# Kernel tuning notes

Hardware: AMD Instinct MI355X
Metric: run time of the kernel (lower is better)

## Reference

```python
import jax, jax.numpy as jnp
import numpy as np

EPS = 1e-7
MAX_NORM = 1.0 - 1e-5  # Poincare ball (c=1) projection radius
NUM_NODES = 50000
NUM_EDGES = 800000
NUM_GRAPHS = 512
D_IN = 64
D_H = 64
D_OUT = 16


def _norm(x):
    return jnp.clip(jnp.linalg.norm(x, axis=-1, keepdims=True), EPS)


def expmap0(u):
    n = _norm(u)
    return jnp.tanh(n) * u / n


def logmap0(x):
    n = _norm(x)
    nc = jnp.clip(n, EPS, MAX_NORM)
    return jnp.arctanh(nc) * x / n


def proj(x):
    n = _norm(x)
    return jnp.where(n > MAX_NORM, x * (MAX_NORM / n), x)


def mobius_add(x, y):
    x2 = jnp.sum(x * x, axis=-1, keepdims=True)
    y2 = jnp.sum(y * y, axis=-1, keepdims=True)
    xy = jnp.sum(x * y, axis=-1, keepdims=True)
    num = (1.0 + 2.0 * xy + y2) * x + (1.0 - x2) * y
    den = jnp.clip(1.0 + 2.0 * xy + x2 * y2, EPS)
    return num / den


def hyp_linear(x, W, b):
    # mobius matvec + hyperbolic bias add
    h = proj(expmap0(logmap0(x) @ W.T))
    hb = proj(expmap0(b))
    return proj(mobius_add(h, hb))


def hyp_agg(x, src, dst, num_nodes):
    # mean aggregation of neighbor messages in the tangent space at the origin
    xt = logmap0(x)                                   # [N, d]
    msg = xt[src]                                     # [E, d] gather
    s = jax.ops.segment_sum(msg, dst, num_segments=num_nodes)
    cnt = jax.ops.segment_sum(jnp.ones((msg.shape[0],), xt.dtype), dst,
                              num_segments=num_nodes)
    agg = s / jnp.clip(cnt, 1.0)[:, None]
    return proj(expmap0(agg))


def hyp_act(x, act):
    return proj(expmap0(act(logmap0(x))))


def hgcn_layer(x, W, b, src, dst, num_nodes, act):
    h = hyp_linear(x, W, b)
    h = hyp_agg(h, src, dst, num_nodes)
    if act is not None:
        h = hyp_act(h, act)
    return h


def setup_inputs() -> dict:
    key = jax.random.key(0)
    ks = jax.random.split(key, 12)
    x = jax.random.normal(ks[0], (NUM_NODES, D_IN), jnp.float32) * 0.1
    edge_index = jax.random.randint(ks[1], (2, NUM_EDGES), 0, NUM_NODES, jnp.int64 if jax.config.jax_enable_x64 else jnp.int32)
    batch = jnp.sort(jax.random.randint(ks[2], (NUM_NODES,), 0, NUM_GRAPHS))
    def w(k, o, i):
        return jax.random.normal(k, (o, i), jnp.float32) * (1.0 / np.sqrt(i))
    return {
        "x": x,
        "W1": w(ks[3], D_H, D_IN), "b1": jnp.zeros((D_H,), jnp.float32),
        "W2": w(ks[4], D_H, D_H),  "b2": jnp.zeros((D_H,), jnp.float32),
        "W3": w(ks[5], D_H, D_H),  "b3": jnp.zeros((D_H,), jnp.float32),
        "W4": w(ks[6], D_OUT, D_H), "b4": jnp.zeros((D_OUT,), jnp.float32),
        "edge_index": edge_index,
        "batch": batch,
    }


def reference(x, W1, b1, W2, b2, W3, b3, W4, b4, edge_index, batch):
    act = lambda v: jax.nn.leaky_relu(v, 0.2)
    n = x.shape[0]
    src, dst = edge_index[0], edge_index[1]
    h = proj(expmap0(x))
    h = hgcn_layer(h, W1, b1, src, dst, n, act)
    h = hgcn_layer(h, W2, b2, src, dst, n, act)
    h = hgcn_layer(h, W3, b3, src, dst, n, None)
    t = logmap0(h)
    # global mean pool over graphs (eval-mode dropout = identity)
    s = jax.ops.segment_sum(t, batch, num_segments=NUM_GRAPHS)
    cnt = jax.ops.segment_sum(jnp.ones((n,), t.dtype), batch, num_segments=NUM_GRAPHS)
    pooled = s / jnp.clip(cnt, 1.0)[:, None]            # [G, d]
    h = proj(expmap0(pooled))
    out = hyp_linear(h, W4, b4)                          # HNNLayer, no activation
    return out
```

## Files before the change

### kernel.cpp

```cpp
#include <hip/hip_runtime.h>
#include <hip/hip_fp16.h>

#define EPSF 1e-7f
#define MAXNORM (1.0f - 1e-5f)

__device__ __forceinline__ float rsum64(float v) {
#pragma unroll
  for (int m = 32; m; m >>= 1) v += __shfl_xor(v, m, 64);
  return v;
}
__device__ __forceinline__ float rsum16(float v) {
#pragma unroll
  for (int m = 8; m; m >>= 1) v += __shfl_xor(v, m, 64);
  return v;
}
__device__ __forceinline__ float gr8(float v) {
  v += __shfl_xor(v, 1, 64);
  v += __shfl_xor(v, 2, 64);
  v += __shfl_xor(v, 4, 64);
  return v;
}

__device__ __forceinline__ float frcp(float x) { return __builtin_amdgcn_rcpf(x); }
__device__ __forceinline__ float fsqrt_(float x) { return __builtin_amdgcn_sqrtf(x); }
__device__ __forceinline__ float tanh_fast(float x) {
  x = fminf(x, 20.f);
  float e = __builtin_amdgcn_exp2f(x * 2.88539008178f);
  return (e - 1.f) * frcp(e + 1.f);
}
__device__ __forceinline__ float atanh_fast(float x) {
  return 0.34657359028f * __builtin_amdgcn_logf((1.f + x) * frcp(1.f - x));
}
__device__ __forceinline__ float lp_exp_log_scale(float nu) {
  float te = tanh_fast(nu);
  float tec = fminf(fmaxf(te, EPSF), MAXNORM);
  return atanh_fast(tec) * frcp(fmaxf(te, EPSF)) * te * frcp(nu);
}

__device__ __forceinline__ float4 ld4(const float* p) {
  return *reinterpret_cast<const float4*>(p);
}

__device__ __forceinline__ void hb_from_b(const float* __restrict__ b, int sub,
                                          float hb8[8], float& hb2) {
  float4 b0 = ld4(b + sub * 8), b1 = ld4(b + sub * 8 + 4);
  float bb8[8] = {b0.x, b0.y, b0.z, b0.w, b1.x, b1.y, b1.z, b1.w};
  float p = 0.f;
#pragma unroll
  for (int j = 0; j < 8; ++j) p = fmaf(bb8[j], bb8[j], p);
  p = gr8(p);
  float nb = fmaxf(fsqrt_(p), EPSF);
  float cb = fminf(tanh_fast(nb), MAXNORM);
  float kb = cb * frcp(nb);
#pragma unroll
  for (int j = 0; j < 8; ++j) hb8[j] = kb * bb8[j];
  hb2 = cb * cb;
}

__device__ __forceinline__ void gather8h(const unsigned short* __restrict__ csr,
                                         const __half* __restrict__ xtp,
                                         int r0, int deg, int g, int sub,
                                         float acc[8]) {
  const uint4* xt4 = reinterpret_cast<const uint4*>(xtp);
  int lb = g << 3;
  int cur = (sub < deg) ? (int)csr[r0 + sub] : 0;
  for (int j0 = 0; j0 < deg; j0 += 8) {
    int nj = j0 + 8;
    int nxt = (nj + sub < deg) ? (int)csr[r0 + nj + sub] : 0;
#pragma unroll
    for (int m = 0; m < 8; ++m) {
      int idx = __shfl(cur, lb + m, 64);
      float msk = (j0 + m < deg) ? 1.f : 0.f;
      union { uint4 u; __half2 h[4]; } U;
      U.u = xt4[(size_t)idx * 8 + sub];
      float2 f0 = __half22float2(U.h[0]);
      float2 f1 = __half22float2(U.h[1]);
      float2 f2 = __half22float2(U.h[2]);
      float2 f3 = __half22float2(U.h[3]);
      acc[0] = fmaf(msk, f0.x, acc[0]); acc[1] = fmaf(msk, f0.y, acc[1]);
      acc[2] = fmaf(msk, f1.x, acc[2]); acc[3] = fmaf(msk, f1.y, acc[3]);
      acc[4] = fmaf(msk, f2.x, acc[4]); acc[5] = fmaf(msk, f2.y, acc[5]);
      acc[6] = fmaf(msk, f3.x, acc[6]); acc[7] = fmaf(msk, f3.y, acc[7]);
    }
    cur = nxt;
  }
}

__device__ __forceinline__ void st8h(__half* __restrict__ xt, int node, int sub,
                                     const float o[8]) {
  union { uint4 u; __half2 h[4]; } U;
  U.h[0] = __floats2half2_rn(o[0], o[1]);
  U.h[1] = __floats2half2_rn(o[2], o[3]);
  U.h[2] = __floats2half2_rn(o[4], o[5]);
  U.h[3] = __floats2half2_rn(o[6], o[7]);
  reinterpret_cast<uint4*>(xt)[(size_t)node * 8 + sub] = U.u;
}

__device__ __forceinline__ void linear_tail8(
    const float* __restrict__ Wl, float* __restrict__ sc, int g, int sub,
    int lane, const float t2[8], const float hb8[8], float hb2, float out8[8]) {
  float4* sw = reinterpret_cast<float4*>(sc + g * 68 + sub * 8);
  sw[0] = make_float4(t2[0], t2[1], t2[2], t2[3]);
  sw[1] = make_float4(t2[4], t2[5], t2[6], t2[7]);
  float y[8] = {0.f, 0.f, 0.f, 0.f, 0.f, 0.f, 0.f, 0.f};
  const float4* Wrow = reinterpret_cast<const float4*>(Wl + lane * 68);
#pragma unroll
  for (int q = 0; q < 16; ++q) {
    float4 w = Wrow[q];
#pragma unroll
    for (int g2 = 0; g2 < 8; ++g2) {
      float4 tq = *reinterpret_cast<const float4*>(sc + g2 * 68 + q * 4);
      y[g2] = fmaf(w.x, tq.x, fmaf(w.y, tq.y, fmaf(w.z, tq.z, fmaf(w.w, tq.w, y[g2]))));
    }
  }
#pragma unroll
  for (int g2 = 0; g2 < 8; ++g2) sc[g2 * 68 + lane] = y[g2];
  float4 r0 = *reinterpret_cast<const float4*>(sc + g * 68 + sub * 8);
  float4 r1 = *reinterpret_cast<const float4*>(sc + g * 68 + sub * 8 + 4);
  float yv[8] = {r0.x, r0.y, r0.z, r0.w, r1.x, r1.y, r1.z, r1.w};
  float p1 = 0.f, p2 = 0.f;
#pragma unroll
  for (int j = 0; j < 8; ++j) {
    p1 = fmaf(yv[j], yv[j], p1);
    p2 = fmaf(yv[j], hb8[j], p2);
  }
  p1 = gr8(p1); p2 = gr8(p2);
  float ny = fmaxf(fsqrt_(p1), EPSF);
  float cy = fminf(tanh_fast(ny), MAXNORM);
  float k = cy * frcp(ny);
  float xy = k * p2;
  float x2 = cy * cy;
  float aa = 1.f + 2.f * xy + hb2;
  float cc = 1.f - x2;
  float den = fmaxf(1.f + 2.f * xy + x2 * hb2, EPSF);
  float rd = frcp(den);
  float nr2 = (aa * aa * x2 + 2.f * aa * cc * xy + cc * cc * hb2) * rd * rd;
  float nr = fmaxf(fsqrt_(nr2), EPSF);
  float s = atanh_fast(fminf(nr, MAXNORM)) * frcp(nr);
  float sk = s * rd;
#pragma unroll
  for (int j = 0; j < 8; ++j) out8[j] = sk * (aa * k * yv[j] + cc * hb8[j]);
}

__global__ void __launch_bounds__(256) k_histg(
    const int* __restrict__ dst, int* __restrict__ deg8, int* __restrict__ rank,
    int E, int N, const int* __restrict__ batch, float* __restrict__ cntg,
    int G, int nbE) {
  if ((int)blockIdx.x < nbE) {
    int e = blockIdx.x * 256 + threadIdx.x;
    if (e >= E) return;
    int c = (e >> 8) & 7;
    rank[e] = atomicAdd(&deg8[(size_t)c * N + dst[e]], 1);
  } else {
    int g = (blockIdx.x - nbE) * 256 + threadIdx.x;
    if (g >= G) return;
    int lo = 0, hi = N;
    while (lo < hi) { int mid = (lo + hi) >> 1; if (batch[mid] < g) lo = mid + 1; else hi = mid; }
    int lb = lo;
    lo = 0; hi = N; int g1 = g + 1;
    while (lo < hi) { int mid = (lo + hi) >> 1; if (batch[mid] < g1) lo = mid + 1; else hi = mid; }
    cntg[g] = (float)(lo - lb);
  }
}

__global__ void __launch_bounds__(256) k_scanAR(const int* __restrict__ deg8,
                                                int* __restrict__ offs8,
                                                int* __restrict__ locscan,
                                                int* __restrict__ partial, int N) {
  __shared__ int buf[256];
  int i = blockIdx.x * 256 + threadIdx.x;
  int s = 0;
  if (i < N) {
#pragma unroll
    for (int k = 0; k < 8; ++k) {
      int v = deg8[(size_t)k * N + i];
      offs8[(size_t)k * N + i] = s;
      s += v;
    }
  }
  int v0 = s;
  buf[threadIdx.x] = v0;
  __syncthreads();
#pragma unroll
  for (int off = 1; off < 256; off <<= 1) {
    int t = (threadIdx.x >= off) ? buf[threadIdx.x - off] : 0;
    __syncthreads();
    buf[threadIdx.x] += t;
    __syncthreads();
  }
  if (i < N) locscan[i] = buf[threadIdx.x] - v0;
  if (threadIdx.x == 255) partial[blockIdx.x] = buf[255];
}

__global__ void __launch_bounds__(256) k_scanB(int* __restrict__ partial, int nb) {
  __shared__ int buf[256];
  int carry = 0;
  for (int base = 0; base < nb; base += 256) {
    int i = base + threadIdx.x;
    int v = (i < nb) ? partial[i] : 0;
    buf[threadIdx.x] = v;
    __syncthreads();
#pragma unroll
    for (int off = 1; off < 256; off <<= 1) {
      int t = (threadIdx.x >= off) ? buf[threadIdx.x - off] : 0;
      __syncthreads();
      buf[threadIdx.x] += t;
      __syncthreads();
    }
    if (i < nb) partial[i] = carry + buf[threadIdx.x] - v;
    int total = buf[255];
    __syncthreads();
    carry += total;
  }
}

__global__ void __launch_bounds__(256) k_scanC(const int* __restrict__ locscan,
                                               const int* __restrict__ partial,
                                               int* __restrict__ rowptr, int N, int E) {
  int i = blockIdx.x * 256 + threadIdx.x;
  if (i < N) rowptr[i] = locscan[i] + partial[blockIdx.x];
  if (i == 0) rowptr[N] = E;
}

__global__ void __launch_bounds__(512) k_filllin(
    const int* __restrict__ src, const int* __restrict__ dst,
    const int* __restrict__ rank, const int* __restrict__ rowptr,
    const int* __restrict__ offs8, unsigned short* __restrict__ csr,
    int E, int N, int nbF,
    const float* __restrict__ x, const float* __restrict__ W,
    const float* __restrict__ b, __half* __restrict__ xt) {
  __shared__ __align__(16) float Wl[64 * 68];
  __shared__ __align__(16) float sc_all[8][8 * 68];
  if ((int)blockIdx.x < nbF) {
    int e = blockIdx.x * 512 + threadIdx.x;
    if (e >= E) return;
    int c = (e >> 8) & 7;
    int d = dst[e];
    csr[rowptr[d] + offs8[(size_t)c * N + d] + rank[e]] = (unsigned short)src[e];
    return;
  }
  int bb = blockIdx.x - nbF;
  int tid = threadIdx.x, wid = tid >> 6, lane = tid & 63;
  int g = lane >> 3, sub = lane & 7;
  for (int i = tid; i < 4096; i += 512) Wl[(i >> 6) * 68 + (i & 63)] = W[i];
  __syncthreads();
  float hb8[8], hb2;
  hb_from_b(b, sub, hb8, hb2);

  int slot = bb * 64 + wid * 8 + g;
  bool valid = slot < N;
  int node = valid ? slot : 0;
  const float* row = x + (size_t)node * 64 + sub * 8;
  float4 v0 = ld4(row), v1 = ld4(row + 4);
  float xa[8] = {v0.x, v0.y, v0.z, v0.w, v1.x, v1.y, v1.z, v1.w};
  float p = 0.f;
#pragma unroll
  for (int j = 0; j < 8; ++j) p = fmaf(xa[j], xa[j], p);
  p = gr8(p);
  float na = fmaxf(fsqrt_(p), EPSF);
  float sc1 = lp_exp_log_scale(na);
  float t2[8];
#pragma unroll
  for (int j = 0; j < 8; ++j) t2[j] = sc1 * xa[j];
  float out8[8];
  linear_tail8(Wl, sc_all[wid], g, sub, lane, t2, hb8, hb2, out8);
  if (valid) st8h(xt, node, sub, out8);
}

__global__ void __launch_bounds__(512) k_gatherlin(
    const int* __restrict__ rowptr, const unsigned short* __restrict__ csr,
    const __half* __restrict__ xtp, const float* __restrict__ W,
    const float* __restrict__ b, __half* __restrict__ xt, int N) {
  __shared__ __align__(16) float Wl[64 * 68];
  __shared__ __align__(16) float sc_all[8][8 * 68];
  int tid = threadIdx.x, wid = tid >> 6, lane = tid & 63;
  int g = lane >> 3, sub = lane & 7;
  for (int i = tid; i < 4096; i += 512) Wl[(i >> 6) * 68 + (i & 63)] = W[i];
  __syncthreads();
  float hb8[8], hb2;
  hb_from_b(b, sub, hb8, hb2);

  int slot = blockIdx.x * 64 + wid * 8 + g;
  bool valid = slot < N;
  int node = valid ? slot : 0;
  int r0 = rowptr[node];
  int deg = valid ? (rowptr[node + 1] - r0) : 0;
  float acc[8] = {0.f, 0.f, 0.f, 0.f, 0.f, 0.f, 0.f, 0.f};
  gather8h(csr, xtp, r0, deg, g, sub, acc);
  float rdeg = frcp(fmaxf((float)deg, 1.f));
  float u[8];
#pragma unroll
  for (int j = 0; j < 8; ++j) u[j] = acc[j] * rdeg;
  float p = 0.f, q = 0.f;
#pragma unroll
  for (int j = 0; j < 8; ++j) {
    float w = (u[j] < 0.f) ? 0.04f : 1.f;
    p = fmaf(u[j], u[j], p);
    q = fmaf(w * u[j], u[j], q);
  }
  p = gr8(p); q = gr8(q);
  float nu = fmaxf(fsqrt_(p), EPSF);
  float s1 = lp_exp_log_scale(nu);
  float nt = fmaxf(s1 * fsqrt_(q), EPSF);
  float f = lp_exp_log_scale(nt) * s1;
  float t2[8];
#pragma unroll
  for (int j = 0; j < 8; ++j) t2[j] = f * u[j] * ((u[j] < 0.f) ? 0.2f : 1.f);
  float out8[8];
  linear_tail8(Wl, sc_all[wid], g, sub, lane, t2, hb8, hb2, out8);
  if (valid) st8h(xt, node, sub, out8);
}

__global__ void __launch_bounds__(512) k_gpool(const int* __restrict__ rowptr,
                                               const unsigned short* __restrict__ csr,
                                               const __half* __restrict__ xtp,
                                               const int* __restrict__ batch,
                                               float* __restrict__ pooled, int N) {
  int tid = threadIdx.x, wid = tid >> 6, lane = tid & 63;
  int g = lane >> 3, sub = lane & 7;
  int slot = blockIdx.x * 64 + wid * 8 + g;
  bool valid = slot < N;
  int node = valid ? slot : 0;
  int r0 = rowptr[node];
  int deg = valid ? (rowptr[node + 1] - r0) : 0;
  float acc[8] = {0.f, 0.f, 0.f, 0.f, 0.f, 0.f, 0.f, 0.f};
  gather8h(csr, xtp, r0, deg, g, sub, acc);
  float rdeg = frcp(fmaxf((float)deg, 1.f));
  float u[8], p = 0.f;
#pragma unroll
  for (int j = 0; j < 8; ++j) {
    u[j] = acc[j] * rdeg;
    p = fmaf(u[j], u[j], p);
  }
  p = gr8(p);
  float nu = fmaxf(fsqrt_(p), EPSF);
  float s = lp_exp_log_scale(nu);
  float t8[8];
#pragma unroll
  for (int j = 0; j < 8; ++j) t8[j] = (valid ? s : 0.f) * u[j];
  int bs = batch[node];
  int b0 = __shfl(bs, 0, 64);
  bool uniform = __all(valid && bs == b0);
  if (uniform) {
#pragma unroll
    for (int j = 0; j < 8; ++j) {
      t8[j] += __shfl_xor(t8[j], 8, 64);
      t8[j] += __shfl_xor(t8[j], 16, 64);
      t8[j] += __shfl_xor(t8[j], 32, 64);
    }
    if (g == 0) {
#pragma unroll
      for (int j = 0; j < 8; ++j)
        atomicAdd(&pooled[(size_t)b0 * 64 + sub * 8 + j], t8[j]);
    }
  } else if (valid) {
#pragma unroll
    for (int j = 0; j < 8; ++j)
      atomicAdd(&pooled[(size_t)bs * 64 + sub * 8 + j], t8[j]);
  }
}

__global__ void __launch_bounds__(64) k_final(const float* __restrict__ pooled,
                                              const float* __restrict__ cntg,
                                              const float* __restrict__ W4,
                                              const float* __restrict__ b4,
                                              float* __restrict__ out, int G) {
  int g = blockIdx.x;
  int lane = threadIdx.x;
  float u = pooled[(size_t)g * 64 + lane] / fmaxf(cntg[g], 1.0f);
  float n = fmaxf(sqrtf(rsum64(u * u)), EPSF);
  float e = tanhf(n) * u / n;
  float ne = fmaxf(sqrtf(rsum64(e * e)), EPSF);
  if (ne > MAXNORM) e *= MAXNORM / ne;
  float nn = fmaxf(sqrtf(rsum64(e * e)), EPSF);
  float t = atanhf(fminf(nn, MAXNORM)) * e / nn;

  int row = lane & 15;
  float acc = 0.f;
#pragma unroll
  for (int k = 0; k < 64; ++k) {
    float tk = __shfl(t, k, 64);
    acc = fmaf(W4[row * 64 + k], tk, acc);
  }
  float ny = fmaxf(sqrtf(rsum16(acc * acc)), EPSF);
  float hy = tanhf(ny) * acc / ny;
  float nh = fmaxf(sqrtf(rsum16(hy * hy)), EPSF);
  if (nh > MAXNORM) hy *= MAXNORM / nh;
  float bb = b4[row];
  float nb = fmaxf(sqrtf(rsum16(bb * bb)), EPSF);
  float hb = tanhf(nb) * bb / nb;
  float nhb = fmaxf(sqrtf(rsum16(hb * hb)), EPSF);
  if (nhb > MAXNORM) hb *= MAXNORM / nhb;
  float x2 = rsum16(hy * hy);
  float y2 = rsum16(hb * hb);
  float xy = rsum16(hy * hb);
  float num = (1.f + 2.f * xy + y2) * hy + (1.f - x2) * hb;
  float den = fmaxf(1.f + 2.f * xy + x2 * y2, EPSF);
  float r = num / den;
  float nr = fmaxf(sqrtf(rsum16(r * r)), EPSF);
  if (nr > MAXNORM) r *= MAXNORM / nr;
  if (lane < 16) out[(size_t)g * 16 + lane] = r;
}

extern "C" void kernel_launch(void* const* d_in, const int* in_sizes, int n_in,
                              void* d_out, int out_size, void* d_ws, size_t ws_size,
                              hipStream_t stream) {
  const float* x  = (const float*)d_in[0];
  const float* W1 = (const float*)d_in[1];
  const float* b1 = (const float*)d_in[2];
  const float* W2 = (const float*)d_in[3];
  const float* b2 = (const float*)d_in[4];
  const float* W3 = (const float*)d_in[5];
  const float* b3 = (const float*)d_in[6];
  const float* W4 = (const float*)d_in[7];
  const float* b4 = (const float*)d_in[8];
  const int* ei   = (const int*)d_in[9];
  const int* batch = (const int*)d_in[10];

  int N = in_sizes[0] / 64;
  int E = in_sizes[9] / 2;
  int G = out_size / 16;
  const int* src = ei;
  const int* dst = ei + E;

  float* ws = (float*)d_ws;
  __half* xtA   = (__half*)ws;
  __half* xtB   = xtA + (size_t)N * 64;
  float* pooled = ws + (size_t)N * 64;
  float* cntg   = pooled + (size_t)G * 64;
  int* ip       = (int*)(cntg + G);
  int* deg8     = ip;
  int* offs8    = deg8 + (size_t)8 * N;
  int* locscan  = offs8 + (size_t)8 * N;
  int* rowptr   = locscan + N;
  int* partial  = rowptr + N + 1;
  int* rank     = partial + 256;
  unsigned short* csr = (unsigned short*)(rank + E);
  float* out = (float*)d_out;

  int nbE = (E + 255) / 256;
  int nbG = (G + 255) / 256;
  int nbN = (N + 255) / 256;
  int nbF = (E + 511) / 512;
  int nbL = (N + 63) / 64;

  hipMemsetAsync(deg8, 0, (size_t)8 * N * sizeof(int), stream);
  hipMemsetAsync(pooled, 0, (size_t)G * 64 * sizeof(float), stream);

  k_histg<<<nbE + nbG, 256, 0, stream>>>(dst, deg8, rank, E, N, batch, cntg, G, nbE);
  k_scanAR<<<nbN, 256, 0, stream>>>(deg8, offs8, locscan, partial, N);
  k_scanB<<<1, 256, 0, stream>>>(partial, nbN);
  k_scanC<<<nbN, 256, 0, stream>>>(locscan, partial, rowptr, N, E);
  k_filllin<<<nbF + nbL, 512, 0, stream>>>(src, dst, rank, rowptr, offs8, csr,
                                           E, N, nbF, x, W1, b1, xtA);
  k_gatherlin<<<nbL, 512, 0, stream>>>(rowptr, csr, xtA, W2, b2, xtB, N);
  k_gatherlin<<<nbL, 512, 0, stream>>>(rowptr, csr, xtB, W3, b3, xtA, N);
  k_gpool<<<nbL, 512, 0, stream>>>(rowptr, csr, xtA, batch, pooled, N);
  k_final<<<G, 64, 0, stream>>>(pooled, cntg, W4, b4, out, G);
}
```

Before: 174.3 us.

## Fuse all pipeline stages into one persistent cooperative kernel with grid syncs

Replaces the nine separate launches and two memsets (histogram, three-stage scan, CSR fill plus first linear, two gather-linear layers, pooling, final head) with a single cooperative kernel. The kernel uses grid-stride loops and grid.sync between stages, and the scan moves to 512-wide blocks. The aim is to remove per-launch overhead and the idle gaps between many small kernels. In exchange, the grid is capped at occupancy, which may reduce parallelism in the gather phases. Each grid barrier has its own cost, and the final head now runs on only a few waves.

```diff
diff --git a/kernel.cpp b/kernel.cpp
--- a/kernel.cpp
+++ b/kernel.cpp
@@ -1,5 +1,8 @@
 #include <hip/hip_runtime.h>
 #include <hip/hip_fp16.h>
+#include <hip/hip_cooperative_groups.h>
+
+namespace cg = cooperative_groups;
 
 #define EPSF 1e-7f
 #define MAXNORM (1.0f - 1e-5f)
@@ -142,286 +145,272 @@
   for (int j = 0; j < 8; ++j) out8[j] = sk * (aa * k * yv[j] + cc * hb8[j]);
 }
 
-__global__ void __launch_bounds__(256) k_histg(
-    const int* __restrict__ dst, int* __restrict__ deg8, int* __restrict__ rank,
-    int E, int N, const int* __restrict__ batch, float* __restrict__ cntg,
-    int G, int nbE) {
-  if ((int)blockIdx.x < nbE) {
-    int e = blockIdx.x * 256 + threadIdx.x;
-    if (e >= E) return;
-    int c = (e >> 8) & 7;
-    rank[e] = atomicAdd(&deg8[(size_t)c * N + dst[e]], 1);
-  } else {
-    int g = (blockIdx.x - nbE) * 256 + threadIdx.x;
-    if (g >= G) return;
-    int lo = 0, hi = N;
-    while (lo < hi) { int mid = (lo + hi) >> 1; if (batch[mid] < g) lo = mid + 1; else hi = mid; }
-    int lb = lo;
-    lo = 0; hi = N; int g1 = g + 1;
-    while (lo < hi) { int mid = (lo + hi) >> 1; if (batch[mid] < g1) lo = mid + 1; else hi = mid; }
-    cntg[g] = (float)(lo - lb);
-  }
-}
-
-__global__ void __launch_bounds__(256) k_scanAR(const int* __restrict__ deg8,
-                                                int* __restrict__ offs8,
-                                                int* __restrict__ locscan,
-                                                int* __restrict__ partial, int N) {
-  __shared__ int buf[256];
-  int i = blockIdx.x * 256 + threadIdx.x;
-  int s = 0;
-  if (i < N) {
-#pragma unroll
-    for (int k = 0; k < 8; ++k) {
-      int v = deg8[(size_t)k * N + i];
-      offs8[(size_t)k * N + i] = s;
-      s += v;
-    }
-  }
-  int v0 = s;
-  buf[threadIdx.x] = v0;
-  __syncthreads();
-#pragma unroll
-  for (int off = 1; off < 256; off <<= 1) {
-    int t = (threadIdx.x >= off) ? buf[threadIdx.x - off] : 0;
-    __syncthreads();
-    buf[threadIdx.x] += t;
-    __syncthreads();
-  }
-  if (i < N) locscan[i] = buf[threadIdx.x] - v0;
-  if (threadIdx.x == 255) partial[blockIdx.x] = buf[255];
-}
-
-__global__ void __launch_bounds__(256) k_scanB(int* __restrict__ partial, int nb) {
-  __shared__ int buf[256];
-  int carry = 0;
-  for (int base = 0; base < nb; base += 256) {
-    int i = base + threadIdx.x;
-    int v = (i < nb) ? partial[i] : 0;
-    buf[threadIdx.x] = v;
-    __syncthreads();
-#pragma unroll
-    for (int off = 1; off < 256; off <<= 1) {
-      int t = (threadIdx.x >= off) ? buf[threadIdx.x - off] : 0;
-      __syncthreads();
-      buf[threadIdx.x] += t;
-      __syncthreads();
-    }
-    if (i < nb) partial[i] = carry + buf[threadIdx.x] - v;
-    int total = buf[255];
-    __syncthreads();
-    carry += total;
-  }
-}
-
-__global__ void __launch_bounds__(256) k_scanC(const int* __restrict__ locscan,
-                                               const int* __restrict__ partial,
-                                               int* __restrict__ rowptr, int N, int E) {
-  int i = blockIdx.x * 256 + threadIdx.x;
-  if (i < N) rowptr[i] = locscan[i] + partial[blockIdx.x];
-  if (i == 0) rowptr[N] = E;
-}
-
-__global__ void __launch_bounds__(512) k_filllin(
-    const int* __restrict__ src, const int* __restrict__ dst,
-    const int* __restrict__ rank, const int* __restrict__ rowptr,
-    const int* __restrict__ offs8, unsigned short* __restrict__ csr,
-    int E, int N, int nbF,
-    const float* __restrict__ x, const float* __restrict__ W,
-    const float* __restrict__ b, __half* __restrict__ xt) {
+struct CoopArgs {
+  const int* src; const int* dst; const int* batch;
+  const float* x;
+  const float* W1; const float* b1;
+  const float* W2; const float* b2;
+  const float* W3; const float* b3;
+  const float* W4; const float* b4;
+  int* deg8; int* offs8; int* locscan; int* rowptr; int* partial;
+  int* rank; unsigned short* csr;
+  __half* xtA; __half* xtB;
+  float* pooled; float* cntg; float* out;
+  int N, E, G;
+};
+
+__global__ void __launch_bounds__(512) k_coop(CoopArgs a) {
+  cg::grid_group grid = cg::this_grid();
   __shared__ __align__(16) float Wl[64 * 68];
   __shared__ __align__(16) float sc_all[8][8 * 68];
-  if ((int)blockIdx.x < nbF) {
-    int e = blockIdx.x * 512 + threadIdx.x;
-    if (e >= E) return;
+  __shared__ int ibuf[512];
+
+  const int tid = threadIdx.x;
+  const int wid = tid >> 6, lane = tid & 63;
+  const int g = lane >> 3, sub = lane & 7;
+  const int gsz = gridDim.x;
+  const int N = a.N, E = a.E, G = a.G;
+  const int gstride = gsz * 512;
+  int gbase = blockIdx.x * 512 + tid;
+
+  for (int i = gbase; i < 8 * N; i += gstride) a.deg8[i] = 0;
+  for (int i = gbase; i < G * 64; i += gstride) a.pooled[i] = 0.f;
+  grid.sync();
+
+  for (int e = gbase; e < E; e += gstride) {
     int c = (e >> 8) & 7;
-    int d = dst[e];
-    csr[rowptr[d] + offs8[(size_t)c * N + d] + rank[e]] = (unsigned short)src[e];
-    return;
-  }
-  int bb = blockIdx.x - nbF;
-  int tid = threadIdx.x, wid = tid >> 6, lane = tid & 63;
-  int g = lane >> 3, sub = lane & 7;
-  for (int i = tid; i < 4096; i += 512) Wl[(i >> 6) * 68 + (i & 63)] = W[i];
+    a.rank[e] = atomicAdd(&a.deg8[(size_t)c * N + a.dst[e]], 1);
+  }
+  for (int gg = gbase; gg < G; gg += gstride) {
+    int lo = 0, hi = N;
+    while (lo < hi) { int mid = (lo + hi) >> 1; if (a.batch[mid] < gg) lo = mid + 1; else hi = mid; }
+    int lb2 = lo;
+    lo = 0; hi = N; int g1 = gg + 1;
+    while (lo < hi) { int mid = (lo + hi) >> 1; if (a.batch[mid] < g1) lo = mid + 1; else hi = mid; }
+    a.cntg[gg] = (float)(lo - lb2);
+  }
+  grid.sync();
+
+  int nbP = (N + 511) / 512;
+  for (int blk = blockIdx.x; blk < nbP; blk += gsz) {
+    int i = blk * 512 + tid;
+    int s = 0;
+    if (i < N) {
+#pragma unroll
+      for (int k = 0; k < 8; ++k) {
+        int v = a.deg8[(size_t)k * N + i];
+        a.offs8[(size_t)k * N + i] = s;
+        s += v;
+      }
+    }
+    int v0 = s;
+    __syncthreads();
+    ibuf[tid] = v0;
+    __syncthreads();
+#pragma unroll
+    for (int off = 1; off < 512; off <<= 1) {
+      int t = (tid >= off) ? ibuf[tid - off] : 0;
+      __syncthreads();
+      ibuf[tid] += t;
+      __syncthreads();
+    }
+    if (i < N) a.locscan[i] = ibuf[tid] - v0;
+    if (tid == 511) a.partial[blk] = ibuf[511];
+  }
+  grid.sync();
+
+  if (blockIdx.x == 0) {
+    int v = (tid < nbP) ? a.partial[tid] : 0;
+    ibuf[tid] = v;
+    __syncthreads();
+#pragma unroll
+    for (int off = 1; off < 512; off <<= 1) {
+      int t = (tid >= off) ? ibuf[tid - off] : 0;
+      __syncthreads();
+      ibuf[tid] += t;
+      __syncthreads();
+    }
+    if (tid < nbP) a.partial[tid] = ibuf[tid] - v;
+  }
+  grid.sync();
+
+  for (int blk = blockIdx.x; blk < nbP; blk += gsz) {
+    int i = blk * 512 + tid;
+    if (i < N) a.rowptr[i] = a.locscan[i] + a.partial[blk];
+  }
+  if (blockIdx.x == 0 && tid == 0) a.rowptr[N] = E;
+  grid.sync();
+
+  for (int e = gbase; e < E; e += gstride) {
+    int c = (e >> 8) & 7;
+    int d = a.dst[e];
+    a.csr[a.rowptr[d] + a.offs8[(size_t)c * N + d] + a.rank[e]] =
+        (unsigned short)a.src[e];
+  }
+  for (int i = tid; i < 4096; i += 512) Wl[(i >> 6) * 68 + (i & 63)] = a.W1[i];
   __syncthreads();
-  float hb8[8], hb2;
-  hb_from_b(b, sub, hb8, hb2);
-
-  int slot = bb * 64 + wid * 8 + g;
-  bool valid = slot < N;
-  int node = valid ? slot : 0;
-  const float* row = x + (size_t)node * 64 + sub * 8;
-  float4 v0 = ld4(row), v1 = ld4(row + 4);
-  float xa[8] = {v0.x, v0.y, v0.z, v0.w, v1.x, v1.y, v1.z, v1.w};
-  float p = 0.f;
-#pragma unroll
-  for (int j = 0; j < 8; ++j) p = fmaf(xa[j], xa[j], p);
-  p = gr8(p);
-  float na = fmaxf(fsqrt_(p), EPSF);
-  float sc1 = lp_exp_log_scale(na);
-  float t2[8];
-#pragma unroll
-  for (int j = 0; j < 8; ++j) t2[j] = sc1 * xa[j];
-  float out8[8];
-  linear_tail8(Wl, sc_all[wid], g, sub, lane, t2, hb8, hb2, out8);
-  if (valid) st8h(xt, node, sub, out8);
-}
-
-__global__ void __launch_bounds__(512) k_gatherlin(
-    const int* __restrict__ rowptr, const unsigned short* __restrict__ csr,
-    const __half* __restrict__ xtp, const float* __restrict__ W,
-    const float* __restrict__ b, __half* __restrict__ xt, int N) {
-  __shared__ __align__(16) float Wl[64 * 68];
-  __shared__ __align__(16) float sc_all[8][8 * 68];
-  int tid = threadIdx.x, wid = tid >> 6, lane = tid & 63;
-  int g = lane >> 3, sub = lane & 7;
-  for (int i = tid; i < 4096; i += 512) Wl[(i >> 6) * 68 + (i & 63)] = W[i];
-  __syncthreads();
-  float hb8[8], hb2;
-  hb_from_b(b, sub, hb8, hb2);
-
-  int slot = blockIdx.x * 64 + wid * 8 + g;
-  bool valid = slot < N;
-  int node = valid ? slot : 0;
-  int r0 = rowptr[node];
-  int deg = valid ? (rowptr[node + 1] - r0) : 0;
-  float acc[8] = {0.f, 0.f, 0.f, 0.f, 0.f, 0.f, 0.f, 0.f};
-  gather8h(csr, xtp, r0, deg, g, sub, acc);
-  float rdeg = frcp(fmaxf((float)deg, 1.f));
-  float u[8];
-#pragma unroll
-  for (int j = 0; j < 8; ++j) u[j] = acc[j] * rdeg;
-  float p = 0.f, q = 0.f;
-#pragma unroll
-  for (int j = 0; j < 8; ++j) {
-    float w = (u[j] < 0.f) ? 0.04f : 1.f;
-    p = fmaf(u[j], u[j], p);
-    q = fmaf(w * u[j], u[j], q);
-  }
-  p = gr8(p); q = gr8(q);
-  float nu = fmaxf(fsqrt_(p), EPSF);
-  float s1 = lp_exp_log_scale(nu);
-  float nt = fmaxf(s1 * fsqrt_(q), EPSF);
-  float f = lp_exp_log_scale(nt) * s1;
-  float t2[8];
-#pragma unroll
-  for (int j = 0; j < 8; ++j) t2[j] = f * u[j] * ((u[j] < 0.f) ? 0.2f : 1.f);
-  float out8[8];
-  linear_tail8(Wl, sc_all[wid], g, sub, lane, t2, hb8, hb2, out8);
-  if (valid) st8h(xt, node, sub, out8);
-}
-
-__global__ void __launch_bounds__(512) k_gpool(const int* __restrict__ rowptr,
-                                               const unsigned short* __restrict__ csr,
-                                               const __half* __restrict__ xtp,
-                                               const int* __restrict__ batch,
-                                               float* __restrict__ pooled, int N) {
-  int tid = threadIdx.x, wid = tid >> 6, lane = tid & 63;
-  int g = lane >> 3, sub = lane & 7;
-  int slot = blockIdx.x * 64 + wid * 8 + g;
-  bool valid = slot < N;
-  int node = valid ? slot : 0;
-  int r0 = rowptr[node];
-  int deg = valid ? (rowptr[node + 1] - r0) : 0;
-  float acc[8] = {0.f, 0.f, 0.f, 0.f, 0.f, 0.f, 0.f, 0.f};
-  gather8h(csr, xtp, r0, deg, g, sub, acc);
-  float rdeg = frcp(fmaxf((float)deg, 1.f));
-  float u[8], p = 0.f;
-#pragma unroll
-  for (int j = 0; j < 8; ++j) {
-    u[j] = acc[j] * rdeg;
-    p = fmaf(u[j], u[j], p);
-  }
-  p = gr8(p);
-  float nu = fmaxf(fsqrt_(p), EPSF);
-  float s = lp_exp_log_scale(nu);
-  float t8[8];
-#pragma unroll
-  for (int j = 0; j < 8; ++j) t8[j] = (valid ? s : 0.f) * u[j];
-  int bs = batch[node];
-  int b0 = __shfl(bs, 0, 64);
-  bool uniform = __all(valid && bs == b0);
-  if (uniform) {
-#pragma unroll
-    for (int j = 0; j < 8; ++j) {
-      t8[j] += __shfl_xor(t8[j], 8, 64);
-      t8[j] += __shfl_xor(t8[j], 16, 64);
-      t8[j] += __shfl_xor(t8[j], 32, 64);
-    }
-    if (g == 0) {
-#pragma unroll
-      for (int j = 0; j < 8; ++j)
-        atomicAdd(&pooled[(size_t)b0 * 64 + sub * 8 + j], t8[j]);
-    }
-  } else if (valid) {
-#pragma unroll
-    for (int j = 0; j < 8; ++j)
-      atomicAdd(&pooled[(size_t)bs * 64 + sub * 8 + j], t8[j]);
-  }
-}
-
-__global__ void __launch_bounds__(64) k_final(const float* __restrict__ pooled,
-                                              const float* __restrict__ cntg,
-                                              const float* __restrict__ W4,
-                                              const float* __restrict__ b4,
-                                              float* __restrict__ out, int G) {
-  int g = blockIdx.x;
-  int lane = threadIdx.x;
-  float u = pooled[(size_t)g * 64 + lane] / fmaxf(cntg[g], 1.0f);
-  float n = fmaxf(sqrtf(rsum64(u * u)), EPSF);
-  float e = tanhf(n) * u / n;
-  float ne = fmaxf(sqrtf(rsum64(e * e)), EPSF);
-  if (ne > MAXNORM) e *= MAXNORM / ne;
-  float nn = fmaxf(sqrtf(rsum64(e * e)), EPSF);
-  float t = atanhf(fminf(nn, MAXNORM)) * e / nn;
-
-  int row = lane & 15;
-  float acc = 0.f;
-#pragma unroll
-  for (int k = 0; k < 64; ++k) {
-    float tk = __shfl(t, k, 64);
-    acc = fmaf(W4[row * 64 + k], tk, acc);
-  }
-  float ny = fmaxf(sqrtf(rsum16(acc * acc)), EPSF);
-  float hy = tanhf(ny) * acc / ny;
-  float nh = fmaxf(sqrtf(rsum16(hy * hy)), EPSF);
-  if (nh > MAXNORM) hy *= MAXNORM / nh;
-  float bb = b4[row];
-  float nb = fmaxf(sqrtf(rsum16(bb * bb)), EPSF);
-  float hb = tanhf(nb) * bb / nb;
-  float nhb = fmaxf(sqrtf(rsum16(hb * hb)), EPSF);
-  if (nhb > MAXNORM) hb *= MAXNORM / nhb;
-  float x2 = rsum16(hy * hy);
-  float y2 = rsum16(hb * hb);
-  float xy = rsum16(hy * hb);
-  float num = (1.f + 2.f * xy + y2) * hy + (1.f - x2) * hb;
-  float den = fmaxf(1.f + 2.f * xy + x2 * y2, EPSF);
-  float r = num / den;
-  float nr = fmaxf(sqrtf(rsum16(r * r)), EPSF);
-  if (nr > MAXNORM) r *= MAXNORM / nr;
-  if (lane < 16) out[(size_t)g * 16 + lane] = r;
+  {
+    float hb8[8], hb2;
+    hb_from_b(a.b1, sub, hb8, hb2);
+    int nbL = (N + 63) / 64;
+    for (int blk = blockIdx.x; blk < nbL; blk += gsz) {
+      int slot = blk * 64 + wid * 8 + g;
+      bool valid = slot < N;
+      int node = valid ? slot : 0;
+      const float* row = a.x + (size_t)node * 64 + sub * 8;
+      float4 v0 = ld4(row), v1 = ld4(row + 4);
+      float xa[8] = {v0.x, v0.y, v0.z, v0.w, v1.x, v1.y, v1.z, v1.w};
+      float p = 0.f;
+#pragma unroll
+      for (int j = 0; j < 8; ++j) p = fmaf(xa[j], xa[j], p);
+      p = gr8(p);
+      float na = fmaxf(fsqrt_(p), EPSF);
+      float sc1 = lp_exp_log_scale(na);
+      float t2[8];
+#pragma unroll
+      for (int j = 0; j < 8; ++j) t2[j] = sc1 * xa[j];
+      float out8[8];
+      linear_tail8(Wl, sc_all[wid], g, sub, lane, t2, hb8, hb2, out8);
+      if (valid) st8h(a.xtA, node, sub, out8);
+    }
+  }
+  grid.sync();
+
+  for (int layer = 0; layer < 2; ++layer) {
+    const float* W = (layer == 0) ? a.W2 : a.W3;
+    const float* b = (layer == 0) ? a.b2 : a.b3;
+    const __half* xin = (layer == 0) ? a.xtA : a.xtB;
+    __half* xout = (layer == 0) ? a.xtB : a.xtA;
+    for (int i = tid; i < 4096; i += 512) Wl[(i >> 6) * 68 + (i & 63)] = W[i];
+    __syncthreads();
+    float hb8[8], hb2;
+    hb_from_b(b, sub, hb8, hb2);
+    int nbL = (N + 63) / 64;
+    for (int blk = blockIdx.x; blk < nbL; blk += gsz) {
+      int slot = blk * 64 + wid * 8 + g;
+      bool valid = slot < N;
+      int node = valid ? slot : 0;
+      int r0 = a.rowptr[node];
+      int deg = valid ? (a.rowptr[node + 1] - r0) : 0;
+      float acc[8] = {0.f, 0.f, 0.f, 0.f, 0.f, 0.f, 0.f, 0.f};
+      gather8h(a.csr, xin, r0, deg, g, sub, acc);
+      float rdeg = frcp(fmaxf((float)deg, 1.f));
+      float u[8];
+#pragma unroll
+      for (int j = 0; j < 8; ++j) u[j] = acc[j] * rdeg;
+      float p = 0.f, q = 0.f;
+#pragma unroll
+      for (int j = 0; j < 8; ++j) {
+        float w = (u[j] < 0.f) ? 0.04f : 1.f;
+        p = fmaf(u[j], u[j], p);
+        q = fmaf(w * u[j], u[j], q);
+      }
+      p = gr8(p); q = gr8(q);
+      float nu = fmaxf(fsqrt_(p), EPSF);
+      float s1 = lp_exp_log_scale(nu);
+      float nt = fmaxf(s1 * fsqrt_(q), EPSF);
+      float f = lp_exp_log_scale(nt) * s1;
+      float t2[8];
+#pragma unroll
+      for (int j = 0; j < 8; ++j) t2[j] = f * u[j] * ((u[j] < 0.f) ? 0.2f : 1.f);
+      float out8[8];
+      linear_tail8(Wl, sc_all[wid], g, sub, lane, t2, hb8, hb2, out8);
+      if (valid) st8h(xout, node, sub, out8);
+    }
+    grid.sync();
+  }
+
+  {
+    int nbL = (N + 63) / 64;
+    for (int blk = blockIdx.x; blk < nbL; blk += gsz) {
+      int slot = blk * 64 + wid * 8 + g;
+      bool valid = slot < N;
+      int node = valid ? slot : 0;
+      int r0 = a.rowptr[node];
+      int deg = valid ? (a.rowptr[node + 1] - r0) : 0;
+      float acc[8] = {0.f, 0.f, 0.f, 0.f, 0.f, 0.f, 0.f, 0.f};
+      gather8h(a.csr, a.xtA, r0, deg, g, sub, acc);
+      float rdeg = frcp(fmaxf((float)deg, 1.f));
+      float u[8], p = 0.f;
+#pragma unroll
+      for (int j = 0; j < 8; ++j) {
+        u[j] = acc[j] * rdeg;
+        p = fmaf(u[j], u[j], p);
+      }
+      p = gr8(p);
+      float nu = fmaxf(fsqrt_(p), EPSF);
+      float s = lp_exp_log_scale(nu);
+      float t8[8];
+#pragma unroll
+      for (int j = 0; j < 8; ++j) t8[j] = (valid ? s : 0.f) * u[j];
+      int bs = a.batch[node];
+      int b0 = __shfl(bs, 0, 64);
+      bool uniform = __all(valid && bs == b0);
+      if (uniform) {
+#pragma unroll
+        for (int j = 0; j < 8; ++j) {
+          t8[j] += __shfl_xor(t8[j], 8, 64);
+          t8[j] += __shfl_xor(t8[j], 16, 64);
+          t8[j] += __shfl_xor(t8[j], 32, 64);
+        }
+        if (g == 0) {
+#pragma unroll
+          for (int j = 0; j < 8; ++j)
+            atomicAdd(&a.pooled[(size_t)b0 * 64 + sub * 8 + j], t8[j]);
+        }
+      } else if (valid) {
+#pragma unroll
+        for (int j = 0; j < 8; ++j)
+          atomicAdd(&a.pooled[(size_t)bs * 64 + sub * 8 + j], t8[j]);
+      }
+    }
+  }
+  grid.sync();
+
+  for (int gi = blockIdx.x * 8 + wid; gi < G; gi += gsz * 8) {
+    float u = a.pooled[(size_t)gi * 64 + lane] / fmaxf(a.cntg[gi], 1.0f);
+    float n = fmaxf(sqrtf(rsum64(u * u)), EPSF);
+    float e = tanhf(n) * u / n;
+    float ne = fmaxf(sqrtf(rsum64(e * e)), EPSF);
+    if (ne > MAXNORM) e *= MAXNORM / ne;
+    float nn = fmaxf(sqrtf(rsum64(e * e)), EPSF);
+    float t = atanhf(fminf(nn, MAXNORM)) * e / nn;
+
+    int row = lane & 15;
+    float acc = 0.f;
+#pragma unroll
+    for (int k = 0; k < 64; ++k) {
+      float tk = __shfl(t, k, 64);
+      acc = fmaf(a.W4[row * 64 + k], tk, acc);
+    }
+    float ny = fmaxf(sqrtf(rsum16(acc * acc)), EPSF);
+    float hy = tanhf(ny) * acc / ny;
+    float nh = fmaxf(sqrtf(rsum16(hy * hy)), EPSF);
+    if (nh > MAXNORM) hy *= MAXNORM / nh;
+    float bb = a.b4[row];
+    float nb = fmaxf(sqrtf(rsum16(bb * bb)), EPSF);
+    float hb = tanhf(nb) * bb / nb;
+    float nhb = fmaxf(sqrtf(rsum16(hb * hb)), EPSF);
+    if (nhb > MAXNORM) hb *= MAXNORM / nhb;
+    float x2 = rsum16(hy * hy);
+    float y2 = rsum16(hb * hb);
+    float xy = rsum16(hy * hb);
+    float num = (1.f + 2.f * xy + y2) * hy + (1.f - x2) * hb;
+    float den = fmaxf(1.f + 2.f * xy + x2 * y2, EPSF);
+    float r = num / den;
+    float nr = fmaxf(sqrtf(rsum16(r * r)), EPSF);
+    if (nr > MAXNORM) r *= MAXNORM / nr;
+    if (lane < 16) a.out[(size_t)gi * 16 + lane] = r;
+  }
 }
 
 extern "C" void kernel_launch(void* const* d_in, const int* in_sizes, int n_in,
                               void* d_out, int out_size, void* d_ws, size_t ws_size,
                               hipStream_t stream) {
-  const float* x  = (const float*)d_in[0];
-  const float* W1 = (const float*)d_in[1];
-  const float* b1 = (const float*)d_in[2];
-  const float* W2 = (const float*)d_in[3];
-  const float* b2 = (const float*)d_in[4];
-  const float* W3 = (const float*)d_in[5];
-  const float* b3 = (const float*)d_in[6];
-  const float* W4 = (const float*)d_in[7];
-  const float* b4 = (const float*)d_in[8];
-  const int* ei   = (const int*)d_in[9];
-  const int* batch = (const int*)d_in[10];
-
   int N = in_sizes[0] / 64;
   int E = in_sizes[9] / 2;
   int G = out_size / 16;
-  const int* src = ei;
-  const int* dst = ei + E;
+  const int* ei = (const int*)d_in[9];
 
   float* ws = (float*)d_ws;
   __half* xtA   = (__half*)ws;
@@ -434,27 +423,33 @@
   int* locscan  = offs8 + (size_t)8 * N;
   int* rowptr   = locscan + N;
   int* partial  = rowptr + N + 1;
-  int* rank     = partial + 256;
+  int* rank     = partial + 512;
   unsigned short* csr = (unsigned short*)(rank + E);
-  float* out = (float*)d_out;
-
-  int nbE = (E + 255) / 256;
-  int nbG = (G + 255) / 256;
-  int nbN = (N + 255) / 256;
-  int nbF = (E + 511) / 512;
+
+  CoopArgs a;
+  a.src = ei; a.dst = ei + E; a.batch = (const int*)d_in[10];
+  a.x = (const float*)d_in[0];
+  a.W1 = (const float*)d_in[1]; a.b1 = (const float*)d_in[2];
+  a.W2 = (const float*)d_in[3]; a.b2 = (const float*)d_in[4];
+  a.W3 = (const float*)d_in[5]; a.b3 = (const float*)d_in[6];
+  a.W4 = (const float*)d_in[7]; a.b4 = (const float*)d_in[8];
+  a.deg8 = deg8; a.offs8 = offs8; a.locscan = locscan; a.rowptr = rowptr;
+  a.partial = partial; a.rank = rank; a.csr = csr;
+  a.xtA = xtA; a.xtB = xtB; a.pooled = pooled; a.cntg = cntg;
+  a.out = (float*)d_out;
+  a.N = N; a.E = E; a.G = G;
+
   int nbL = (N + 63) / 64;
-
-  hipMemsetAsync(deg8, 0, (size_t)8 * N * sizeof(int), stream);
-  hipMemsetAsync(pooled, 0, (size_t)G * 64 * sizeof(float), stream);
-
-  k_histg<<<nbE + nbG, 256, 0, stream>>>(dst, deg8, rank, E, N, batch, cntg, G, nbE);
-  k_scanAR<<<nbN, 256, 0, stream>>>(deg8, offs8, locscan, partial, N);
-  k_scanB<<<1, 256, 0, stream>>>(partial, nbN);
-  k_scanC<<<nbN, 256, 0, stream>>>(locscan, partial, rowptr, N, E);
-  k_filllin<<<nbF + nbL, 512, 0, stream>>>(src, dst, rank, rowptr, offs8, csr,
-                                           E, N, nbF, x, W1, b1, xtA);
-  k_gatherlin<<<nbL, 512, 0, stream>>>(rowptr, csr, xtA, W2, b2, xtB, N);
-  k_gatherlin<<<nbL, 512, 0, stream>>>(rowptr, csr, xtB, W3, b3, xtA, N);
-  k_gpool<<<nbL, 512, 0, stream>>>(rowptr, csr, xtA, batch, pooled, N);
-  k_final<<<G, 64, 0, stream>>>(pooled, cntg, W4, b4, out, G);
-}
+  int perCU = 0;
+  hipOccupancyMaxActiveBlocksPerMultiprocessor(&perCU, k_coop, 512, 0);
+  if (perCU < 1) perCU = 1;
+  int dev = 0, numCU = 256;
+  hipGetDevice(&dev);
+  hipDeviceGetAttribute(&numCU, hipDeviceAttributeMultiprocessorCount, dev);
+  int cap = perCU * numCU;
+  int grid = (nbL < cap) ? nbL : cap;
+
+  void* params[] = {&a};
+  hipLaunchCooperativeKernel((const void*)k_coop, dim3(grid), dim3(512),
+                             params, 0, stream);
+}
```

Measured after the change: 440.9 us. +152.9%, slower.

## Fuse three-pass CSR scan into one kernel with last-block completion

Applied to the files above, without the earlier changes.

Replaces the three scan kernels (block scan, partial scan, add-back) with one 512-thread kernel. The last block to finish, found through an atomic counter, scans the block partials and writes rowptr for all nodes. It also zeroes the pooled buffer, so the separate memset for it goes away and the counter's zeroing rides on the existing deg8 memset. This cuts two kernel launches and one memset, but the final rowptr write is now done serially by a single block over all N nodes.

```diff
diff --git a/kernel.cpp b/kernel.cpp
--- a/kernel.cpp
+++ b/kernel.cpp
@@ -163,12 +163,17 @@
   }
 }
 
-__global__ void __launch_bounds__(256) k_scanAR(const int* __restrict__ deg8,
-                                                int* __restrict__ offs8,
-                                                int* __restrict__ locscan,
-                                                int* __restrict__ partial, int N) {
-  __shared__ int buf[256];
-  int i = blockIdx.x * 256 + threadIdx.x;
+__global__ void __launch_bounds__(512) k_scanR(
+    const int* __restrict__ deg8, int* __restrict__ offs8,
+    int* __restrict__ locscan, int* __restrict__ rowptr,
+    int* __restrict__ partial, int* __restrict__ done,
+    float* __restrict__ pooled, int N, int E, int PG) {
+  __shared__ int ibuf[512];
+  __shared__ int amlast;
+  int nbP = (int)gridDim.x;
+  int tid = threadIdx.x;
+  int blk = blockIdx.x;
+  int i = blk * 512 + tid;
   int s = 0;
   if (i < N) {
 #pragma unroll
@@ -179,47 +184,39 @@
     }
   }
   int v0 = s;
-  buf[threadIdx.x] = v0;
-  __syncthreads();
-#pragma unroll
-  for (int off = 1; off < 256; off <<= 1) {
-    int t = (threadIdx.x >= off) ? buf[threadIdx.x - off] : 0;
+  ibuf[tid] = v0;
+  __syncthreads();
+#pragma unroll
+  for (int off = 1; off < 512; off <<= 1) {
+    int t = (tid >= off) ? ibuf[tid - off] : 0;
     __syncthreads();
-    buf[threadIdx.x] += t;
+    ibuf[tid] += t;
     __syncthreads();
   }
-  if (i < N) locscan[i] = buf[threadIdx.x] - v0;
-  if (threadIdx.x == 255) partial[blockIdx.x] = buf[255];
-}
-
-__global__ void __launch_bounds__(256) k_scanB(int* __restrict__ partial, int nb) {
-  __shared__ int buf[256];
-  int carry = 0;
-  for (int base = 0; base < nb; base += 256) {
-    int i = base + threadIdx.x;
-    int v = (i < nb) ? partial[i] : 0;
-    buf[threadIdx.x] = v;
+  if (i < N) locscan[i] = ibuf[tid] - v0;
+  if (tid == 511) partial[blk] = ibuf[511];
+  __threadfence();
+  __syncthreads();
+  if (tid == 0) amlast = (atomicAdd(done, 1) == nbP - 1) ? 1 : 0;
+  __syncthreads();
+  if (!amlast) return;
+  __threadfence();
+  int pv = (tid < nbP) ? partial[tid] : 0;
+  ibuf[tid] = pv;
+  __syncthreads();
+#pragma unroll
+  for (int off = 1; off < 512; off <<= 1) {
+    int t = (tid >= off) ? ibuf[tid - off] : 0;
     __syncthreads();
-#pragma unroll
-    for (int off = 1; off < 256; off <<= 1) {
-      int t = (threadIdx.x >= off) ? buf[threadIdx.x - off] : 0;
-      __syncthreads();
-      buf[threadIdx.x] += t;
-      __syncthreads();
-    }
-    if (i < nb) partial[i] = carry + buf[threadIdx.x] - v;
-    int total = buf[255];
+    ibuf[tid] += t;
     __syncthreads();
-    carry += total;
-  }
-}
-
-__global__ void __launch_bounds__(256) k_scanC(const int* __restrict__ locscan,
-                                               const int* __restrict__ partial,
-                                               int* __restrict__ rowptr, int N, int E) {
-  int i = blockIdx.x * 256 + threadIdx.x;
-  if (i < N) rowptr[i] = locscan[i] + partial[blockIdx.x];
-  if (i == 0) rowptr[N] = E;
+  }
+  if (tid < nbP) partial[tid] = ibuf[tid] - pv;
+  __syncthreads();
+  for (int j = tid; j < N; j += 512)
+    rowptr[j] = locscan[j] + partial[j >> 9];
+  if (tid == 0) rowptr[N] = E;
+  for (int j = tid; j < PG; j += 512) pooled[j] = 0.f;
 }
 
 __global__ void __launch_bounds__(512) k_filllin(
@@ -430,27 +427,26 @@
   float* cntg   = pooled + (size_t)G * 64;
   int* ip       = (int*)(cntg + G);
   int* deg8     = ip;
-  int* offs8    = deg8 + (size_t)8 * N;
+  int* done     = deg8 + (size_t)8 * N;
+  int* offs8    = done + 16;
   int* locscan  = offs8 + (size_t)8 * N;
   int* rowptr   = locscan + N;
   int* partial  = rowptr + N + 1;
-  int* rank     = partial + 256;
+  int* rank     = partial + 512;
   unsigned short* csr = (unsigned short*)(rank + E);
   float* out = (float*)d_out;
 
   int nbE = (E + 255) / 256;
   int nbG = (G + 255) / 256;
-  int nbN = (N + 255) / 256;
+  int nbP = (N + 511) / 512;
   int nbF = (E + 511) / 512;
   int nbL = (N + 63) / 64;
 
-  hipMemsetAsync(deg8, 0, (size_t)8 * N * sizeof(int), stream);
-  hipMemsetAsync(pooled, 0, (size_t)G * 64 * sizeof(float), stream);
+  hipMemsetAsync(deg8, 0, ((size_t)8 * N + 16) * sizeof(int), stream);
 
   k_histg<<<nbE + nbG, 256, 0, stream>>>(dst, deg8, rank, E, N, batch, cntg, G, nbE);
-  k_scanAR<<<nbN, 256, 0, stream>>>(deg8, offs8, locscan, partial, N);
-  k_scanB<<<1, 256, 0, stream>>>(partial, nbN);
-  k_scanC<<<nbN, 256, 0, stream>>>(locscan, partial, rowptr, N, E);
+  k_scanR<<<nbP, 512, 0, stream>>>(deg8, offs8, locscan, rowptr, partial, done,
+                                   pooled, N, E, G * 64);
   k_filllin<<<nbF + nbL, 512, 0, stream>>>(src, dst, rank, rowptr, offs8, csr,
                                            E, N, nbF, x, W1, b1, xtA);
   k_gatherlin<<<nbL, 512, 0, stream>>>(rowptr, csr, xtA, W2, b2, xtB, N);
```

Measured after the change: 201.5 us. 15.6% more time.
